# Optimization experiments

Hardware: AMD Instinct MI355X
Metric: run time of the kernel (lower is better)

Reference implementation:

```python
import jax, jax.numpy as jnp
import numpy as np

ALIGNED_H, ALIGNED_W = 7, 7          # module init args
AH, AW = ALIGNED_H + 1, ALIGNED_W + 1  # RoIAlignFunction sampling grid (8x8)


def setup_inputs() -> dict:
    key = jax.random.key(0)
    k1, k2, k3, k4 = jax.random.split(key, 4)
    B, C, H, W = 4, 256, 200, 200
    N = 1024
    spatial_scale = jnp.float32(1.0 / 16.0)
    img = H / (1.0 / 16.0)  # 3200 px image-space extent
    features = jax.random.normal(k1, (B, C, H, W), dtype=jnp.float32)
    bidx = jax.random.randint(k2, (N,), 0, B).astype(jnp.float32)
    xy1 = jax.random.uniform(k3, (N, 2), minval=0.0, maxval=img - 64.0)
    wh = jax.random.uniform(k4, (N, 2), minval=16.0, maxval=512.0)
    xy2 = jnp.minimum(xy1 + wh, img - 1.0)
    rois = jnp.concatenate(
        [bidx[:, None], xy1[:, 0:1], xy1[:, 1:2], xy2[:, 0:1], xy2[:, 1:2]], axis=1
    ).astype(jnp.float32)
    return {"features": features, "rois": rois, "spatial_scale": spatial_scale}


def _roi_align(features, rois, spatial_scale):
    B, C, H, W = features.shape
    b = rois[:, 0].astype(jnp.int32)
    x1 = rois[:, 1] * spatial_scale
    y1 = rois[:, 2] * spatial_scale
    x2 = rois[:, 3] * spatial_scale
    y2 = rois[:, 4] * spatial_scale
    bin_h = jnp.maximum(y2 - y1 + 1.0, 0.0) / (AH - 1)   # [N]
    bin_w = jnp.maximum(x2 - x1 + 1.0, 0.0) / (AW - 1)
    ph = jnp.arange(AH, dtype=features.dtype)
    pw = jnp.arange(AW, dtype=features.dtype)
    h = y1[:, None] + ph * bin_h[:, None]                 # [N, AH] sample rows
    w = x1[:, None] + pw * bin_w[:, None]                 # [N, AW] sample cols
    hs_f = jnp.minimum(jnp.floor(h), H - 2.0)             # clip as in CUDA kernel
    ws_f = jnp.minimum(jnp.floor(w), W - 2.0)
    hr = h - hs_f                                         # bilinear ratios
    wr = w - ws_f
    hi = jnp.clip(hs_f, 0.0, None).astype(jnp.int32)      # safe gather indices
    wi = jnp.clip(ws_f, 0.0, None).astype(jnp.int32)
    valid = ((h >= 0) & (h < H))[:, :, None] & ((w >= 0) & (w < W))[:, None, :]
    bb = b[:, None, None]
    Hg = hi[:, :, None]
    Wg = wi[:, None, :]

    def g(dh, dw):
        # advanced-index gather -> [N, AH, AW, C]
        return features[bb, :, Hg + dh, Wg + dw]

    hr_ = hr[:, :, None, None]
    wr_ = wr[:, None, :, None]
    val = (g(0, 0) * (1 - hr_) * (1 - wr_)
           + g(0, 1) * (1 - hr_) * wr_
           + g(1, 0) * hr_ * (1 - wr_)
           + g(1, 1) * hr_ * wr_)
    val = jnp.where(valid[..., None], val, 0.0)
    return jnp.transpose(val, (0, 3, 1, 2))               # [N, C, AH, AW]


def reference(features, rois, spatial_scale):
    x = _roi_align(features, rois, spatial_scale)
    # avg_pool2d(kernel_size=2, stride=1): 8x8 -> 7x7
    return (x[:, :, :-1, :-1] + x[:, :, :-1, 1:]
            + x[:, :, 1:, :-1] + x[:, :, 1:, 1:]) * 0.25
```

## Files before the change

kernel.cpp:

```cpp
#include <hip/hip_runtime.h>

#define BATCH 4
#define CH    256
#define FH    200
#define FW    200
#define NROI  1024
#define PLANE (FH * FW)
#define POOL  7
#define NWAVE 16

__global__ __launch_bounds__(1024) void build_roi_lists(
    const float* __restrict__ rois, int* __restrict__ cnt, int* __restrict__ idx)
{
    __shared__ int lcnt[BATCH];
    const int tid = threadIdx.x;
    if (tid < BATCH) lcnt[tid] = 0;
    __syncthreads();
    const int b = (int)rois[tid * 5];
    const int pos = atomicAdd(&lcnt[b], 1);
    idx[(b << 10) + pos] = tid;
    __syncthreads();
    if (tid < BATCH) cnt[tid] = lcnt[tid];
}

__global__ __launch_bounds__(1024, 1) void roialign_lds_kernel(
    const float* __restrict__ feat,
    const float* __restrict__ rois,
    const float* __restrict__ scale_p,
    const int*   __restrict__ cnt,
    const int*   __restrict__ idx,
    float* __restrict__ out)
{
    __shared__ float splane[PLANE];

    const int c   = blockIdx.x;
    const int b   = blockIdx.y;
    const int tid = threadIdx.x;

    {
        const float4* __restrict__ src =
            (const float4*)(feat + ((size_t)b * CH + c) * PLANE);
        float4* dst = (float4*)splane;
        for (int i = tid; i < PLANE / 4; i += 1024)
            dst[i] = src[i];
    }
    __syncthreads();

    const float scale = scale_p[0];
    const int wave = tid >> 6;
    const int lane = tid & 63;
    const int ph   = lane >> 3;
    const int pw   = lane & 7;
    const bool do_store = (ph < POOL) && (pw < POOL);

    const int cntb = __builtin_amdgcn_readfirstlane(cnt[b]);

#pragma unroll 2
    for (int i = wave; i < cntb; i += NWAVE) {
        int n = idx[(b << 10) + i];
        n = __builtin_amdgcn_readfirstlane(n);

        const float x1 = rois[n * 5 + 1] * scale;
        const float y1 = rois[n * 5 + 2] * scale;
        const float x2 = rois[n * 5 + 3] * scale;
        const float y2 = rois[n * 5 + 4] * scale;

        const float bin_h = fmaxf(y2 - y1 + 1.0f, 0.0f) * (1.0f / 7.0f);
        const float bin_w = fmaxf(x2 - x1 + 1.0f, 0.0f) * (1.0f / 7.0f);

        const float h    = y1 + (float)ph * bin_h;
        const float w    = x1 + (float)pw * bin_w;
        const float hs_f = fminf(floorf(h), (float)(FH - 2));
        const float ws_f = fminf(floorf(w), (float)(FW - 2));
        const float hr   = h - hs_f;
        const float wr   = w - ws_f;
        const int   hi   = (int)fmaxf(hs_f, 0.0f);
        const int   wi   = (int)fmaxf(ws_f, 0.0f);
        const bool  valid = (h >= 0.0f) && (h < (float)FH) &&
                            (w >= 0.0f) && (w < (float)FW);
        const float m = valid ? 0.25f : 0.0f;

        const float w00 = (1.0f - hr) * (1.0f - wr) * m;
        const float w01 = (1.0f - hr) * wr * m;
        const float w10 = hr * (1.0f - wr) * m;
        const float w11 = hr * wr * m;

        const int off = hi * FW + wi;
        const float g00 = splane[off];
        const float g01 = splane[off + 1];
        const float g10 = splane[off + FW];
        const float g11 = splane[off + FW + 1];

        float v  = g00 * w00 + g01 * w01 + g10 * w10 + g11 * w11;

        float s1 = v + __shfl_down(v, 1, 64);
        float s2 = s1 + __shfl_down(s1, 8, 64);

        if (do_store)
            __builtin_nontemporal_store(
                s2, out + ((size_t)n * CH + c) * (POOL * POOL) + ph * POOL + pw);
    }
}

#define CGROUPS 8
#define CH_PER_WAVE 8
__global__ __launch_bounds__(256) void roialign_gather_kernel(
    const float* __restrict__ feat, const float* __restrict__ rois,
    const float* __restrict__ scale_p, float* __restrict__ out)
{
    const int n = blockIdx.x, g = blockIdx.y, tid = threadIdx.x;
    const int wave = tid >> 6, lane = tid & 63;
    const int ph = lane >> 3, pw = lane & 7;
    const float scale = scale_p[0];
    const int   b  = (int)rois[n * 5 + 0];
    const float x1 = rois[n * 5 + 1] * scale, y1 = rois[n * 5 + 2] * scale;
    const float x2 = rois[n * 5 + 3] * scale, y2 = rois[n * 5 + 4] * scale;
    const float bin_h = fmaxf(y2 - y1 + 1.0f, 0.0f) / 7.0f;
    const float bin_w = fmaxf(x2 - x1 + 1.0f, 0.0f) / 7.0f;
    const float h = y1 + (float)ph * bin_h, w = x1 + (float)pw * bin_w;
    const float hs_f = fminf(floorf(h), (float)(FH - 2));
    const float ws_f = fminf(floorf(w), (float)(FW - 2));
    const float hr = h - hs_f, wr = w - ws_f;
    const int hi = (int)fmaxf(hs_f, 0.0f), wi = (int)fmaxf(ws_f, 0.0f);
    const bool valid = (h >= 0.0f) && (h < (float)FH) && (w >= 0.0f) && (w < (float)FW);
    const float m = valid ? 0.25f : 0.0f;
    const float w00 = (1.0f - hr) * (1.0f - wr) * m, w01 = (1.0f - hr) * wr * m;
    const float w10 = hr * (1.0f - wr) * m, w11 = hr * wr * m;
    const int c0 = g * (4 * CH_PER_WAVE) + wave * CH_PER_WAVE;
    const float* p = feat + ((size_t)(b * CH + c0)) * PLANE + (size_t)(hi * FW + wi);
    float* outp = out + ((size_t)n * CH + c0) * (POOL * POOL) + ph * POOL + pw;
    const bool do_store = (ph < POOL) && (pw < POOL);
#pragma unroll
    for (int dc = 0; dc < CH_PER_WAVE; ++dc) {
        float v = p[0] * w00 + p[1] * w01 + p[FW] * w10 + p[FW + 1] * w11;
        float s1 = v + __shfl_down(v, 1, 64);
        float s2 = s1 + __shfl_down(s1, 8, 64);
        if (do_store) __builtin_nontemporal_store(s2, outp);
        p += PLANE; outp += POOL * POOL;
    }
}

extern "C" void kernel_launch(void* const* d_in, const int* in_sizes, int n_in,
                              void* d_out, int out_size, void* d_ws, size_t ws_size,
                              hipStream_t stream) {
    const float* feat    = (const float*)d_in[0];
    const float* rois    = (const float*)d_in[1];
    const float* scale_p = (const float*)d_in[2];
    float*       out     = (float*)d_out;
    (void)in_sizes; (void)n_in; (void)out_size;

    const size_t ws_needed = (size_t)(BATCH + BATCH * NROI) * sizeof(int);
    if (ws_size >= ws_needed) {
        int* cnt = (int*)d_ws;
        int* idx = cnt + BATCH;
        hipLaunchKernelGGL(build_roi_lists, dim3(1), dim3(1024), 0, stream,
                           rois, cnt, idx);
        hipLaunchKernelGGL(roialign_lds_kernel, dim3(CH, BATCH), dim3(1024), 0,
                           stream, feat, rois, scale_p, cnt, idx, out);
    } else {
        hipLaunchKernelGGL(roialign_gather_kernel, dim3(NROI, CGROUPS), dim3(256),
                           0, stream, feat, rois, scale_p, out);
    }
}
```

Before: 273.1 us.

## Replace LDS plane staging with XCD-aware L2-resident channel-set gather kernel

```diff
diff --git a/kernel.cpp b/kernel.cpp
--- a/kernel.cpp
+++ b/kernel.cpp
@@ -7,7 +7,10 @@
 #define NROI  1024
 #define PLANE (FH * FW)
 #define POOL  7
-#define NWAVE 16
+#define NCG   16
+#define CHPW  4
+#define SLOTS 256
+#define NSETS (BATCH * NCG)
 
 __global__ __launch_bounds__(1024) void build_roi_lists(
     const float* __restrict__ rois, int* __restrict__ cnt, int* __restrict__ idx)
@@ -23,7 +26,7 @@
     if (tid < BATCH) cnt[tid] = lcnt[tid];
 }
 
-__global__ __launch_bounds__(1024, 1) void roialign_lds_kernel(
+__global__ __launch_bounds__(256) void roialign_l2set_kernel(
     const float* __restrict__ feat,
     const float* __restrict__ rois,
     const float* __restrict__ scale_p,
@@ -31,34 +34,27 @@
     const int*   __restrict__ idx,
     float* __restrict__ out)
 {
-    __shared__ float splane[PLANE];
+    const int bid = blockIdx.x;
+    const int xcd = bid & 7;
+    const int j   = bid >> 3;
+    const int s   = xcd + 8 * (j >> 8);
+    const int w   = j & 255;
+    const int b   = s >> 4;
+    const int g   = s & 15;
 
-    const int c   = blockIdx.x;
-    const int b   = blockIdx.y;
-    const int tid = threadIdx.x;
-
-    {
-        const float4* __restrict__ src =
-            (const float4*)(feat + ((size_t)b * CH + c) * PLANE);
-        float4* dst = (float4*)splane;
-        for (int i = tid; i < PLANE / 4; i += 1024)
-            dst[i] = src[i];
-    }
-    __syncthreads();
-
-    const float scale = scale_p[0];
+    const int tid  = threadIdx.x;
     const int wave = tid >> 6;
     const int lane = tid & 63;
     const int ph   = lane >> 3;
     const int pw   = lane & 7;
     const bool do_store = (ph < POOL) && (pw < POOL);
 
+    const float scale = scale_p[0];
     const int cntb = __builtin_amdgcn_readfirstlane(cnt[b]);
+    const int c0   = (g << 4) + (wave << 2);
 
-#pragma unroll 2
-    for (int i = wave; i < cntb; i += NWAVE) {
-        int n = idx[(b << 10) + i];
-        n = __builtin_amdgcn_readfirstlane(n);
+    for (int w0 = w; w0 < cntb; w0 += SLOTS) {
+        const int n = __builtin_amdgcn_readfirstlane(idx[(b << 10) + w0]);
 
         const float x1 = rois[n * 5 + 1] * scale;
         const float y1 = rois[n * 5 + 2] * scale;
@@ -69,15 +65,15 @@
         const float bin_w = fmaxf(x2 - x1 + 1.0f, 0.0f) * (1.0f / 7.0f);
 
         const float h    = y1 + (float)ph * bin_h;
-        const float w    = x1 + (float)pw * bin_w;
+        const float ww   = x1 + (float)pw * bin_w;
         const float hs_f = fminf(floorf(h), (float)(FH - 2));
-        const float ws_f = fminf(floorf(w), (float)(FW - 2));
+        const float ws_f = fminf(floorf(ww), (float)(FW - 2));
         const float hr   = h - hs_f;
-        const float wr   = w - ws_f;
+        const float wr   = ww - ws_f;
         const int   hi   = (int)fmaxf(hs_f, 0.0f);
         const int   wi   = (int)fmaxf(ws_f, 0.0f);
         const bool  valid = (h >= 0.0f) && (h < (float)FH) &&
-                            (w >= 0.0f) && (w < (float)FW);
+                            (ww >= 0.0f) && (ww < (float)FW);
         const float m = valid ? 0.25f : 0.0f;
 
         const float w00 = (1.0f - hr) * (1.0f - wr) * m;
@@ -85,20 +81,31 @@
         const float w10 = hr * (1.0f - wr) * m;
         const float w11 = hr * wr * m;
 
-        const int off = hi * FW + wi;
-        const float g00 = splane[off];
-        const float g01 = splane[off + 1];
-        const float g10 = splane[off + FW];
-        const float g11 = splane[off + FW + 1];
+        const float* p = feat + ((size_t)(b * CH + c0)) * PLANE
+                              + (size_t)(hi * FW + wi);
+        float* outp = out + ((size_t)n * CH + c0) * (POOL * POOL)
+                          + ph * POOL + pw;
 
-        float v  = g00 * w00 + g01 * w01 + g10 * w10 + g11 * w11;
+        float g00[CHPW], g01[CHPW], g10[CHPW], g11[CHPW];
+#pragma unroll
+        for (int dc = 0; dc < CHPW; ++dc) {
+            const float* q = p + (size_t)dc * PLANE;
+            g00[dc] = q[0];
+            g01[dc] = q[1];
+            g10[dc] = q[FW];
+            g11[dc] = q[FW + 1];
+        }
+        __builtin_amdgcn_sched_barrier(0);
 
-        float s1 = v + __shfl_down(v, 1, 64);
-        float s2 = s1 + __shfl_down(s1, 8, 64);
-
-        if (do_store)
-            __builtin_nontemporal_store(
-                s2, out + ((size_t)n * CH + c) * (POOL * POOL) + ph * POOL + pw);
+#pragma unroll
+        for (int dc = 0; dc < CHPW; ++dc) {
+            float v  = g00[dc] * w00 + g01[dc] * w01
+                     + g10[dc] * w10 + g11[dc] * w11;
+            float s1 = v + __shfl_down(v, 1, 64);
+            float s2 = s1 + __shfl_down(s1, 8, 64);
+            if (do_store)
+                __builtin_nontemporal_store(s2, outp + dc * (POOL * POOL));
+        }
     }
 }
 
@@ -155,8 +162,8 @@
         int* idx = cnt + BATCH;
         hipLaunchKernelGGL(build_roi_lists, dim3(1), dim3(1024), 0, stream,
                            rois, cnt, idx);
-        hipLaunchKernelGGL(roialign_lds_kernel, dim3(CH, BATCH), dim3(1024), 0,
-                           stream, feat, rois, scale_p, cnt, idx, out);
+        hipLaunchKernelGGL(roialign_l2set_kernel, dim3(NSETS * SLOTS), dim3(256),
+                           0, stream, feat, rois, scale_p, cnt, idx, out);
     } else {
         hipLaunchKernelGGL(roialign_gather_kernel, dim3(NROI, CGROUPS), dim3(256),
                            0, stream, feat, rois, scale_p, out);
```

Result: faster. 266.9 us (-2.3%).

## Precompute per-ROI bilinear offsets and weights once, pad LDS rows

Applied to the files above, without the earlier changes.

```diff
diff --git a/kernel.cpp b/kernel.cpp
--- a/kernel.cpp
+++ b/kernel.cpp
@@ -7,31 +7,84 @@
 #define NROI  1024
 #define PLANE (FH * FW)
 #define POOL  7
+#define SAMP  8
 #define NWAVE 16
+#define LSTRIDE 204
 
-__global__ __launch_bounds__(1024) void build_roi_lists(
-    const float* __restrict__ rois, int* __restrict__ cnt, int* __restrict__ idx)
+#define WS_CNT 0
+#define WS_IDX 4
+#define WS_OFF (4 + BATCH * NROI)
+#define WS_W4_BYTE ((size_t)(WS_OFF + BATCH * NROI * 64) * 4)
+#define WS_NEEDED (WS_W4_BYTE + (size_t)BATCH * NROI * 64 * 16)
+
+__global__ __launch_bounds__(64) void precompute_kernel(
+    const float* __restrict__ rois, const float* __restrict__ scale_p,
+    int* __restrict__ ws_i, float4* __restrict__ w4)
 {
-    __shared__ int lcnt[BATCH];
-    const int tid = threadIdx.x;
-    if (tid < BATCH) lcnt[tid] = 0;
-    __syncthreads();
-    const int b = (int)rois[tid * 5];
-    const int pos = atomicAdd(&lcnt[b], 1);
-    idx[(b << 10) + pos] = tid;
-    __syncthreads();
-    if (tid < BATCH) cnt[tid] = lcnt[tid];
+    const int n    = blockIdx.x;
+    const int lane = threadIdx.x;
+    const int ph   = lane >> 3;
+    const int pw   = lane & 7;
+
+    const int b_n = (int)rois[n * 5];
+
+    int before = 0, total = 0;
+    for (int k = 0; k < NROI / 64; ++k) {
+        const int j  = (k << 6) + lane;
+        const int bj = (int)rois[j * 5];
+        const unsigned long long mask = __ballot(bj == b_n);
+        total += __popcll(mask);
+        const int lim = n - (k << 6);
+        if (lim > 0) {
+            const unsigned long long mm =
+                (lim >= 64) ? mask : (mask & ((1ull << lim) - 1ull));
+            before += __popcll(mm);
+        }
+    }
+    const int slot = before;
+    if (lane == 0) {
+        ws_i[WS_IDX + (b_n << 10) + slot] = n;
+        if (slot == 0) ws_i[WS_CNT + b_n] = total;
+    }
+
+    const float scale = scale_p[0];
+    const float x1 = rois[n * 5 + 1] * scale;
+    const float y1 = rois[n * 5 + 2] * scale;
+    const float x2 = rois[n * 5 + 3] * scale;
+    const float y2 = rois[n * 5 + 4] * scale;
+    const float bin_h = fmaxf(y2 - y1 + 1.0f, 0.0f) * (1.0f / 7.0f);
+    const float bin_w = fmaxf(x2 - x1 + 1.0f, 0.0f) * (1.0f / 7.0f);
+
+    const float h    = y1 + (float)ph * bin_h;
+    const float w    = x1 + (float)pw * bin_w;
+    const float hs_f = fminf(floorf(h), (float)(FH - 2));
+    const float ws_f = fminf(floorf(w), (float)(FW - 2));
+    const float hr   = h - hs_f;
+    const float wr   = w - ws_f;
+    const int   hi   = (int)fmaxf(hs_f, 0.0f);
+    const int   wi   = (int)fmaxf(ws_f, 0.0f);
+    const bool  valid = (h >= 0.0f) && (h < (float)FH) &&
+                        (w >= 0.0f) && (w < (float)FW);
+    const float m = valid ? 0.25f : 0.0f;
+
+    float4 wv;
+    wv.x = (1.0f - hr) * (1.0f - wr) * m;
+    wv.y = (1.0f - hr) * wr * m;
+    wv.z = hr * (1.0f - wr) * m;
+    wv.w = hr * wr * m;
+
+    const int rec = (((b_n << 10) + slot) << 6) + lane;
+    ws_i[WS_OFF + rec] = hi * LSTRIDE + wi;
+    w4[rec] = wv;
 }
 
-__global__ __launch_bounds__(1024, 1) void roialign_lds_kernel(
+__global__ __launch_bounds__(1024, 1) void roialign_lds2_kernel(
     const float* __restrict__ feat,
-    const float* __restrict__ rois,
-    const float* __restrict__ scale_p,
-    const int*   __restrict__ cnt,
-    const int*   __restrict__ idx,
+    const int*   __restrict__ ws_i,
+    const float4* __restrict__ w4,
     float* __restrict__ out)
 {
-    __shared__ float splane[PLANE];
+    __shared__ float splane[LSTRIDE * FH];
 
     const int c   = blockIdx.x;
     const int b   = blockIdx.y;
@@ -40,58 +93,37 @@
     {
         const float4* __restrict__ src =
             (const float4*)(feat + ((size_t)b * CH + c) * PLANE);
-        float4* dst = (float4*)splane;
-        for (int i = tid; i < PLANE / 4; i += 1024)
-            dst[i] = src[i];
+        for (int j = tid; j < PLANE / 4; j += 1024) {
+            const int row = j / 50;
+            const int col = (j - row * 50) << 2;
+            *(float4*)&splane[row * LSTRIDE + col] = src[j];
+        }
     }
     __syncthreads();
 
-    const float scale = scale_p[0];
     const int wave = tid >> 6;
     const int lane = tid & 63;
     const int ph   = lane >> 3;
     const int pw   = lane & 7;
     const bool do_store = (ph < POOL) && (pw < POOL);
 
-    const int cntb = __builtin_amdgcn_readfirstlane(cnt[b]);
+    int cntb = __builtin_amdgcn_readfirstlane(ws_i[WS_CNT + b]);
+    cntb = (cntb > NROI) ? NROI : cntb;
 
 #pragma unroll 2
     for (int i = wave; i < cntb; i += NWAVE) {
-        int n = idx[(b << 10) + i];
-        n = __builtin_amdgcn_readfirstlane(n);
+        const int n   = __builtin_amdgcn_readfirstlane(ws_i[WS_IDX + (b << 10) + i]);
+        const int rec = (((b << 10) + i) << 6) + lane;
 
-        const float x1 = rois[n * 5 + 1] * scale;
-        const float y1 = rois[n * 5 + 2] * scale;
-        const float x2 = rois[n * 5 + 3] * scale;
-        const float y2 = rois[n * 5 + 4] * scale;
+        const int    off = ws_i[WS_OFF + rec];
+        const float4 wv  = w4[rec];
 
-        const float bin_h = fmaxf(y2 - y1 + 1.0f, 0.0f) * (1.0f / 7.0f);
-        const float bin_w = fmaxf(x2 - x1 + 1.0f, 0.0f) * (1.0f / 7.0f);
-
-        const float h    = y1 + (float)ph * bin_h;
-        const float w    = x1 + (float)pw * bin_w;
-        const float hs_f = fminf(floorf(h), (float)(FH - 2));
-        const float ws_f = fminf(floorf(w), (float)(FW - 2));
-        const float hr   = h - hs_f;
-        const float wr   = w - ws_f;
-        const int   hi   = (int)fmaxf(hs_f, 0.0f);
-        const int   wi   = (int)fmaxf(ws_f, 0.0f);
-        const bool  valid = (h >= 0.0f) && (h < (float)FH) &&
-                            (w >= 0.0f) && (w < (float)FW);
-        const float m = valid ? 0.25f : 0.0f;
-
-        const float w00 = (1.0f - hr) * (1.0f - wr) * m;
-        const float w01 = (1.0f - hr) * wr * m;
-        const float w10 = hr * (1.0f - wr) * m;
-        const float w11 = hr * wr * m;
-
-        const int off = hi * FW + wi;
         const float g00 = splane[off];
         const float g01 = splane[off + 1];
-        const float g10 = splane[off + FW];
-        const float g11 = splane[off + FW + 1];
+        const float g10 = splane[off + LSTRIDE];
+        const float g11 = splane[off + LSTRIDE + 1];
 
-        float v  = g00 * w00 + g01 * w01 + g10 * w10 + g11 * w11;
+        float v  = g00 * wv.x + g01 * wv.y + g10 * wv.z + g11 * wv.w;
 
         float s1 = v + __shfl_down(v, 1, 64);
         float s2 = s1 + __shfl_down(s1, 8, 64);
@@ -149,14 +181,13 @@
     float*       out     = (float*)d_out;
     (void)in_sizes; (void)n_in; (void)out_size;
 
-    const size_t ws_needed = (size_t)(BATCH + BATCH * NROI) * sizeof(int);
-    if (ws_size >= ws_needed) {
-        int* cnt = (int*)d_ws;
-        int* idx = cnt + BATCH;
-        hipLaunchKernelGGL(build_roi_lists, dim3(1), dim3(1024), 0, stream,
-                           rois, cnt, idx);
-        hipLaunchKernelGGL(roialign_lds_kernel, dim3(CH, BATCH), dim3(1024), 0,
-                           stream, feat, rois, scale_p, cnt, idx, out);
+    if (ws_size >= WS_NEEDED) {
+        int*    ws_i = (int*)d_ws;
+        float4* w4   = (float4*)((char*)d_ws + WS_W4_BYTE);
+        hipLaunchKernelGGL(precompute_kernel, dim3(NROI), dim3(64), 0, stream,
+                           rois, scale_p, ws_i, w4);
+        hipLaunchKernelGGL(roialign_lds2_kernel, dim3(CH, BATCH), dim3(1024), 0,
+                           stream, feat, ws_i, w4, out);
     } else {
         hipLaunchKernelGGL(roialign_gather_kernel, dim3(NROI, CGROUPS), dim3(256),
                            0, stream, feat, rois, scale_p, out);
```

Measured after the change: 273.5 us. About the same (+0.1%).
